# Optimization experiments

Measured on AMD Instinct MI355X. Metric: run time of the kernel, lower is better.

The kernel has to match this reference:

```python
import jax, jax.numpy as jnp
import numpy as np

N_NODES = 100000
N_EDGES = 1600000
IN_CH = 64
HID = 64
OUT = 2


def sage_conv(x, src, dst, W_agg, W_root, b):
    # PyG SAGEConv (mean aggr): out = lin_l(mean_{j in N(i)} x_j) + lin_r(x_i)
    n = x.shape[0]
    msgs = x[src]                                        # [E, F] gather
    agg = jax.ops.segment_sum(msgs, dst, num_segments=n)  # [N, F] scatter-add
    cnt = jax.ops.segment_sum(jnp.ones((src.shape[0], 1), x.dtype), dst, num_segments=n)
    agg = agg / jnp.maximum(cnt, 1)                      # mean; isolated nodes -> 0
    return agg @ W_agg + x @ W_root + b


def setup_inputs() -> dict:
    key = jax.random.key(0)
    ks = jax.random.split(key, 8)
    s = lambda f: 1.0 / np.sqrt(f)
    x = jax.random.normal(ks[0], (N_NODES, IN_CH), dtype=jnp.float32)
    edge_index = jax.random.randint(ks[1], (2, N_EDGES), 0, N_NODES, dtype=jnp.int64)
    return {
        "x": x,
        "edge_index": edge_index,
        "W1_agg": jax.random.normal(ks[2], (IN_CH, HID), dtype=jnp.float32) * s(IN_CH),
        "W1_root": jax.random.normal(ks[3], (IN_CH, HID), dtype=jnp.float32) * s(IN_CH),
        "b1": jnp.zeros((HID,), jnp.float32),
        "W2_agg": jax.random.normal(ks[4], (HID, HID), dtype=jnp.float32) * s(HID),
        "W2_root": jax.random.normal(ks[5], (HID, HID), dtype=jnp.float32) * s(HID),
        "b2": jnp.zeros((HID,), jnp.float32),
        "W_lin": jax.random.normal(ks[6], (HID, OUT), dtype=jnp.float32) * s(HID),
        "b_lin": jnp.zeros((OUT,), jnp.float32),
    }


def reference(x, edge_index, W1_agg, W1_root, b1, W2_agg, W2_root, b2, W_lin, b_lin):
    src, dst = edge_index[0], edge_index[1]
    h = jax.nn.relu(sage_conv(x, src, dst, W1_agg, W1_root, b1))   # dropout = identity (eval)
    h = jax.nn.relu(sage_conv(h, src, dst, W2_agg, W2_root, b2))
    return h @ W_lin + b_lin
```

## Files before the change

kernel.cpp:

```cpp
#include <hip/hip_runtime.h>
#include <hip/hip_bf16.h>

#define FEAT 64
#define CHUNK 8192
#define MAX_NB 1024

typedef __attribute__((ext_vector_type(8))) short bf16x8;
typedef __attribute__((ext_vector_type(4))) float f32x4;

__device__ __forceinline__ float bflo2f(unsigned int u) {
    union { unsigned int u; float f; } v; v.u = u << 16; return v.f;
}
__device__ __forceinline__ float bfhi2f(unsigned int u) {
    union { unsigned int u; float f; } v; v.u = u & 0xffff0000u; return v.f;
}
__device__ __forceinline__ unsigned short f2bf(float f) {
    union { float f; unsigned int u; } v; v.f = f;
    unsigned int u = v.u;
    u += 0x7fffu + ((u >> 16) & 1u);
    return (unsigned short)(u >> 16);
}

__global__ void detect_kernel(const unsigned short* __restrict__ xh,
                              const int* __restrict__ ei32,
                              int* __restrict__ flags) {
    __shared__ int cnt_bf, cnt_nz;
    int tid = threadIdx.x;
    if (tid == 0) { cnt_bf = 0; cnt_nz = 0; }
    __syncthreads();
    unsigned short h = xh[tid * 2];
    int e = (h >> 7) & 0xFF;
    if (e >= 110 && e <= 132) atomicAdd(&cnt_bf, 1);
    if (ei32[tid * 2 + 1] != 0) atomicAdd(&cnt_nz, 1);
    __syncthreads();
    if (tid == 0) {
        flags[0] = (cnt_bf >= 128) ? 1 : 0;
        flags[1] = (cnt_nz < 8) ? 1 : 0;
    }
}

__global__ void cvt_x_kernel(const void* __restrict__ in, unsigned short* __restrict__ out16,
                             int n8, const int* __restrict__ flags) {
    int i = blockIdx.x * 256 + threadIdx.x;
    if (i >= n8) return;
    if (flags[0]) {
        ((uint4*)out16)[i] = ((const uint4*)in)[i];
    } else {
        float4 a = ((const float4*)in)[2 * i];
        float4 b = ((const float4*)in)[2 * i + 1];
        uint4 o;
        o.x = (unsigned int)f2bf(a.x) | ((unsigned int)f2bf(a.y) << 16);
        o.y = (unsigned int)f2bf(a.z) | ((unsigned int)f2bf(a.w) << 16);
        o.z = (unsigned int)f2bf(b.x) | ((unsigned int)f2bf(b.y) << 16);
        o.w = (unsigned int)f2bf(b.z) | ((unsigned int)f2bf(b.w) << 16);
        ((uint4*)out16)[i] = o;
    }
}

__global__ void cvt_weights_kernel(const void* __restrict__ w1a, const void* __restrict__ w1r,
                                   const void* __restrict__ b1,  const void* __restrict__ w2a,
                                   const void* __restrict__ w2r, const void* __restrict__ b2,
                                   const void* __restrict__ wl,  const void* __restrict__ bl,
                                   float* __restrict__ out, unsigned short* __restrict__ Wt,
                                   const int* __restrict__ flags) {
    int i = blockIdx.x * 256 + threadIdx.x;
    if (i >= 16642) return;
    const void* src; int off;
    if      (i < 4096)  { src = w1a; off = i; }
    else if (i < 8192)  { src = w1r; off = i - 4096; }
    else if (i < 8256)  { src = b1;  off = i - 8192; }
    else if (i < 12352) { src = w2a; off = i - 8256; }
    else if (i < 16448) { src = w2r; off = i - 12352; }
    else if (i < 16512) { src = b2;  off = i - 16448; }
    else if (i < 16640) { src = wl;  off = i - 16512; }
    else                { src = bl;  off = i - 16640; }
    float v = flags[0] ? bflo2f(((const unsigned short*)src)[off])
                       : ((const float*)src)[off];
    out[i] = v;
    unsigned short hv = f2bf(v);
    if (i < 4096)                      Wt[(off & 63) * 128 + (off >> 6)] = hv;
    else if (i < 8192)                 Wt[(off & 63) * 128 + 64 + (off >> 6)] = hv;
    else if (i >= 8256 && i < 12352)   Wt[8192 + (off & 63) * 128 + (off >> 6)] = hv;
    else if (i >= 12352 && i < 16448)  Wt[8192 + (off & 63) * 128 + 64 + (off >> 6)] = hv;
}

__global__ __launch_bounds__(256) void p1_hist_kernel(
    const int* __restrict__ ei32, int* __restrict__ hist,
    int E, int N, int NB, int EC, const int* __restrict__ flags) {
    __shared__ int lh[MAX_NB];
    int tid = threadIdx.x, c = blockIdx.x;
    for (int i = tid; i < NB; i += 256) lh[i] = 0;
    __syncthreads();
    int idx64 = flags[1];
    long base = (long)c * CHUNK;
#pragma unroll 4
    for (int j = 0; j < CHUNK / 256; ++j) {
        long e = base + j * 256 + tid;
        if (e < E) {
            int s = idx64 ? ei32[2 * e]             : ei32[e];
            int d = idx64 ? ei32[2 * ((long)E + e)] : ei32[(long)E + e];
            if ((unsigned)s < (unsigned)N && (unsigned)d < (unsigned)N)
                atomicAdd(&lh[d >> 8], 1);
        }
    }
    __syncthreads();
    for (int k = tid; k < NB; k += 256) hist[(long)k * EC + c] = lh[k];
}

__global__ __launch_bounds__(256) void scan1_kernel(const int* __restrict__ in,
                                                    int* __restrict__ out,
                                                    int* __restrict__ blocksum, int n) {
    int tid = threadIdx.x;
    int base = blockIdx.x * 2048 + tid * 8;
    int v[8];
    int tsum = 0;
#pragma unroll
    for (int i = 0; i < 8; ++i) {
        v[i] = (base + i < n) ? in[base + i] : 0;
        tsum += v[i];
    }
    int lane = tid & 63;
    int x = tsum;
#pragma unroll
    for (int off = 1; off < 64; off <<= 1) {
        int y = __shfl_up(x, off);
        if (lane >= off) x += y;
    }
    __shared__ int wsum[4];
    int wave = tid >> 6;
    if (lane == 63) wsum[wave] = x;
    __syncthreads();
    int woff = 0;
#pragma unroll
    for (int w = 0; w < 4; ++w) if (w < wave) woff += wsum[w];
    int run = woff + x - tsum;
#pragma unroll
    for (int i = 0; i < 8; ++i) {
        if (base + i < n) out[base + i] = run;
        run += v[i];
    }
    if (tid == 255) blocksum[blockIdx.x] = woff + x;
}

__global__ void scan2_kernel(int* __restrict__ blocksum, int B) {
    if (threadIdx.x == 0 && blockIdx.x == 0) {
        int run = 0;
        for (int i = 0; i < B; ++i) { int v = blocksum[i]; blocksum[i] = run; run += v; }
    }
}

__global__ void scan3_kernel(int* __restrict__ out, const int* __restrict__ blocksum, int n) {
    int i = blockIdx.x * 256 + threadIdx.x;
    if (i < n) out[i] += blocksum[i >> 11];
}

__global__ __launch_bounds__(256) void p3_scatter_kernel(
    const int* __restrict__ ei32, const int* __restrict__ hscan,
    int* __restrict__ bkt, int E, int N, int NB, int EC,
    const int* __restrict__ flags) {
    __shared__ int lh[MAX_NB];
    int tid = threadIdx.x, c = blockIdx.x;
    for (int i = tid; i < NB; i += 256) lh[i] = 0;
    __syncthreads();
    int idx64 = flags[1];
    long base = (long)c * CHUNK;
#pragma unroll 4
    for (int j = 0; j < CHUNK / 256; ++j) {
        long e = base + j * 256 + tid;
        if (e < E) {
            int s = idx64 ? ei32[2 * e]             : ei32[e];
            int d = idx64 ? ei32[2 * ((long)E + e)] : ei32[(long)E + e];
            if ((unsigned)s < (unsigned)N && (unsigned)d < (unsigned)N) {
                int k = d >> 8;
                int r = atomicAdd(&lh[k], 1);
                bkt[hscan[(long)k * EC + c] + r] = s | ((d & 255) << 20);
            }
        }
    }
}

__global__ __launch_bounds__(256) void p4_build_kernel(
    const int* __restrict__ bkt, const int* __restrict__ hscan, const int* __restrict__ hist,
    int* __restrict__ offs, int* __restrict__ cnt, int* __restrict__ srcs,
    int E, int N, int NB, int EC) {
    int k = blockIdx.x, tid = threadIdx.x;
    int start = hscan[(long)k * EC];
    int end = (k + 1 < NB) ? hscan[(long)(k + 1) * EC]
                           : (hscan[(long)NB * EC - 1] + hist[(long)NB * EC - 1]);
    __shared__ int lc[256], lheads[256], wsum[4];
    lc[tid] = 0;
    __syncthreads();
    for (int e = start + tid; e < end; e += 256)
        atomicAdd(&lc[(bkt[e] >> 20) & 255], 1);
    __syncthreads();
    int cv = lc[tid];
    int lane = tid & 63, wave = tid >> 6;
    int x = cv;
#pragma unroll
    for (int off = 1; off < 64; off <<= 1) {
        int y = __shfl_up(x, off);
        if (lane >= off) x += y;
    }
    if (lane == 63) wsum[wave] = x;
    __syncthreads();
    int woff = 0;
#pragma unroll
    for (int w = 0; w < 4; ++w) if (w < wave) woff += wsum[w];
    int excl = woff + x - cv;
    int gnode = k * 256 + tid;
    if (gnode < N) { offs[gnode] = start + excl; cnt[gnode] = cv; }
    lheads[tid] = excl;
    __syncthreads();
    for (int e = start + tid; e < end; e += 256) {
        int p = bkt[e];
        int d8 = (p >> 20) & 255;
        int pos = start + atomicAdd(&lheads[d8], 1);
        srcs[pos] = p & 0xFFFFF;
    }
}

__global__ __launch_bounds__(256) void aggregate_kernel(
    const unsigned short* __restrict__ feat16, const int* __restrict__ srcs,
    const int* __restrict__ offs, const int* __restrict__ cnt,
    unsigned short* __restrict__ agg16, int N) {
    long gid = (long)blockIdx.x * 256 + threadIdx.x;
    int node = (int)(gid >> 6);
    if (node >= N) return;
    int lane = threadIdx.x & 63;
    int half = lane >> 5;
    int li = lane & 31;
    int start = offs[node];
    int deg = cnt[node];
    int end = start + deg;
    float acc0 = 0.f, acc1 = 0.f;
    int e = start;
    for (; e + 8 <= end; e += 8) {
        int s0 = srcs[e + 0 + half];
        int s1 = srcs[e + 2 + half];
        int s2 = srcs[e + 4 + half];
        int s3 = srcs[e + 6 + half];
        unsigned u0 = *(const unsigned*)(feat16 + (size_t)s0 * FEAT + 2 * li);
        unsigned u1 = *(const unsigned*)(feat16 + (size_t)s1 * FEAT + 2 * li);
        unsigned u2 = *(const unsigned*)(feat16 + (size_t)s2 * FEAT + 2 * li);
        unsigned u3 = *(const unsigned*)(feat16 + (size_t)s3 * FEAT + 2 * li);
        acc0 += bflo2f(u0 & 0xffffu); acc1 += bfhi2f(u0);
        acc0 += bflo2f(u1 & 0xffffu); acc1 += bfhi2f(u1);
        acc0 += bflo2f(u2 & 0xffffu); acc1 += bfhi2f(u2);
        acc0 += bflo2f(u3 & 0xffffu); acc1 += bfhi2f(u3);
    }
    for (; e < end; e += 2) {
        int idx = e + half;
        int s = srcs[idx < end ? idx : end - 1];
        unsigned u = *(const unsigned*)(feat16 + (size_t)s * FEAT + 2 * li);
        if (idx < end) { acc0 += bflo2f(u & 0xffffu); acc1 += bfhi2f(u); }
    }
    acc0 += __shfl_xor(acc0, 32);
    acc1 += __shfl_xor(acc1, 32);
    if (half == 0) {
        float inv = 1.0f / (float)(deg > 0 ? deg : 1);
        unsigned o = (unsigned)f2bf(acc0 * inv) | ((unsigned)f2bf(acc1 * inv) << 16);
        *(unsigned*)(agg16 + (size_t)node * FEAT + 2 * li) = o;
    }
}

__global__ __launch_bounds__(256) void sage_gemm_kernel(
    const unsigned short* __restrict__ agg16, const unsigned short* __restrict__ root16,
    const unsigned short* __restrict__ Wt, const float* __restrict__ bias,
    unsigned short* __restrict__ out16, int N,
    const float* __restrict__ wl, const float* __restrict__ bl,
    void* __restrict__ out_final, const int* __restrict__ flags) {

    __shared__ unsigned short A_l[64][136];
    __shared__ unsigned short B_l[64][136];

    int tid = threadIdx.x;
    int blk = blockIdx.x;

#pragma unroll
    for (int i = 0; i < 4; ++i) {
        int ch = tid + i * 256;
        int n = ch >> 4, kc = ch & 15;
        *(uint4*)&B_l[n][kc * 8] = *(const uint4*)(Wt + n * 128 + kc * 8);
    }
#pragma unroll
    for (int i = 0; i < 4; ++i) {
        int ch = tid + i * 256;
        int r = ch >> 4, c = ch & 15;
        int row = blk * 64 + r;
        uint4 u = make_uint4(0, 0, 0, 0);
        if (row < N)
            u = (c < 8) ? ((const uint4*)(agg16 + (size_t)row * FEAT))[c]
                        : ((const uint4*)(root16 + (size_t)row * FEAT))[c - 8];
        *(uint4*)&A_l[r][c * 8] = u;
    }
    __syncthreads();

    int lane = tid & 63;
    int wave = tid >> 6;
    int r0 = wave * 16;
    int m = lane & 15, quad = lane >> 4;

    f32x4 acc0 = {0.f, 0.f, 0.f, 0.f};
    f32x4 acc1 = acc0, acc2 = acc0, acc3 = acc0;

#pragma unroll
    for (int k0 = 0; k0 < 128; k0 += 32) {
        bf16x8 a = *(const bf16x8*)&A_l[r0 + m][k0 + quad * 8];
        bf16x8 b0 = *(const bf16x8*)&B_l[ 0 + m][k0 + quad * 8];
        bf16x8 b1 = *(const bf16x8*)&B_l[16 + m][k0 + quad * 8];
        bf16x8 b2 = *(const bf16x8*)&B_l[32 + m][k0 + quad * 8];
        bf16x8 b3 = *(const bf16x8*)&B_l[48 + m][k0 + quad * 8];
        acc0 = __builtin_amdgcn_mfma_f32_16x16x32_bf16(a, b0, acc0, 0, 0, 0);
        acc1 = __builtin_amdgcn_mfma_f32_16x16x32_bf16(a, b1, acc1, 0, 0, 0);
        acc2 = __builtin_amdgcn_mfma_f32_16x16x32_bf16(a, b2, acc2, 0, 0, 0);
        acc3 = __builtin_amdgcn_mfma_f32_16x16x32_bf16(a, b3, acc3, 0, 0, 0);
    }
    __syncthreads();

#pragma unroll
    for (int c = 0; c < 4; ++c) {
        f32x4 av = (c == 0) ? acc0 : (c == 1) ? acc1 : (c == 2) ? acc2 : acc3;
        float bv = bias[c * 16 + m];
#pragma unroll
        for (int reg = 0; reg < 4; ++reg) {
            float v = fmaxf(av[reg] + bv, 0.f);
            A_l[r0 + quad * 4 + reg][c * 16 + m] = f2bf(v);
        }
    }
    __syncthreads();

#pragma unroll
    for (int i = 0; i < 2; ++i) {
        int ch = tid + i * 256;
        int r = ch >> 3, c = ch & 7;
        int row = blk * 64 + r;
        if (row < N)
            ((uint4*)(out16 + (size_t)row * FEAT))[c] = *(const uint4*)&A_l[r][c * 8];
    }

    if (wl) {
        int r = tid >> 2, part = tid & 3;
        int row = blk * 64 + r;
        if (row < N) {
            float p0 = 0.f, p1 = 0.f;
#pragma unroll
            for (int j = 0; j < 16; ++j) {
                int f = part * 16 + j;
                float v = bflo2f(A_l[r][f]);
                p0 += v * wl[f * 2 + 0];
                p1 += v * wl[f * 2 + 1];
            }
            p0 += __shfl_down(p0, 2, 4); p0 += __shfl_down(p0, 1, 4);
            p1 += __shfl_down(p1, 2, 4); p1 += __shfl_down(p1, 1, 4);
            if (part == 0) {
                p0 += bl[0];
                p1 += bl[1];
                if (flags[0]) {
                    unsigned int o = ((unsigned int)f2bf(p1) << 16) | (unsigned int)f2bf(p0);
                    ((unsigned int*)out_final)[row] = o;
                } else {
                    ((float2*)out_final)[row] = make_float2(p0, p1);
                }
            }
        }
    }
}

extern "C" void kernel_launch(void* const* d_in, const int* in_sizes, int n_in,
                              void* d_out, int out_size, void* d_ws, size_t ws_size,
                              hipStream_t stream) {
    const void* x_in = d_in[0];
    const int*  ei32 = (const int*)d_in[1];

    int N = in_sizes[0] / FEAT;
    int E = in_sizes[1] / 2;
    int NB = (N + 255) >> 8;
    int EC = (E + CHUNK - 1) / CHUNK;
    int HN = NB * EC;

    unsigned short* x16   = (unsigned short*)d_ws;
    unsigned short* h16   = x16 + (size_t)N * FEAT;
    unsigned short* agg16 = h16 + (size_t)N * FEAT;
    unsigned short* Wt    = agg16 + (size_t)N * FEAT;
    float*          wbuf  = (float*)(Wt + 16384);
    int*            hist  = (int*)(wbuf + 16704);
    int*            hscan = hist + HN;
    int*            bsum  = hscan + HN;
    int*            flags = bsum + 1024;
    int*            offs  = flags + 16;
    int*            cnt   = offs + N;
    int*            bkt   = cnt + N;
    int*            srcs  = bkt + E;

    float* b1_32 = wbuf + 8192;
    float* b2_32 = wbuf + 16448;
    float* wl32  = wbuf + 16512;
    float* bl32  = wbuf + 16640;

    detect_kernel<<<1, 256, 0, stream>>>((const unsigned short*)x_in, ei32, flags);

    int n8 = N * FEAT / 8;
    cvt_x_kernel<<<(n8 + 255) / 256, 256, 0, stream>>>(x_in, x16, n8, flags);
    cvt_weights_kernel<<<(16642 + 255) / 256, 256, 0, stream>>>(
        d_in[2], d_in[3], d_in[4], d_in[5], d_in[6], d_in[7], d_in[8], d_in[9],
        wbuf, Wt, flags);

    p1_hist_kernel<<<EC, 256, 0, stream>>>(ei32, hist, E, N, NB, EC, flags);
    int sB = (HN + 2047) / 2048;
    scan1_kernel<<<sB, 256, 0, stream>>>(hist, hscan, bsum, HN);
    scan2_kernel<<<1, 64, 0, stream>>>(bsum, sB);
    scan3_kernel<<<(HN + 255) / 256, 256, 0, stream>>>(hscan, bsum, HN);
    p3_scatter_kernel<<<EC, 256, 0, stream>>>(ei32, hscan, bkt, E, N, NB, EC, flags);
    p4_build_kernel<<<NB, 256, 0, stream>>>(bkt, hscan, hist, offs, cnt, srcs, E, N, NB, EC);

    int aBlocks = (int)(((long)N * 64 + 255) / 256);
    int gBlocks = (N + 63) / 64;

    aggregate_kernel<<<aBlocks, 256, 0, stream>>>(x16, srcs, offs, cnt, agg16, N);
    sage_gemm_kernel<<<gBlocks, 256, 0, stream>>>(agg16, x16, Wt, b1_32, h16, N,
                                                  nullptr, nullptr, nullptr, flags);

    aggregate_kernel<<<aBlocks, 256, 0, stream>>>(h16, srcs, offs, cnt, agg16, N);
    sage_gemm_kernel<<<gBlocks, 256, 0, stream>>>(agg16, h16, Wt + 8192, b2_32, h16, N,
                                                  wl32, bl32, d_out, flags);
}
```

Measured before the change: 282.1 us.

## Vectorize neighbor gather to 16-byte loads and drop redundant prepasses

The aggregate kernel now gives each lane eight bf16 features through one 16-byte load, with eight edges in flight per wave instead of two, and reduces across lane groups with shuffles. The bf16-input path no longer copies x into a workspace and reads the raw input directly. The histogram pass stops loading source indices, and the single-thread scan2 launch is folded into scan3 as a per-thread prefix loop over block sums. Invalid source indices are clamped to 0 rather than dropped, which changes the semantics for out-of-range edges, and scan3 repeats the block-sum reads in every thread.

```diff
diff --git a/kernel.cpp b/kernel.cpp
--- a/kernel.cpp
+++ b/kernel.cpp
@@ -41,20 +41,17 @@
 
 __global__ void cvt_x_kernel(const void* __restrict__ in, unsigned short* __restrict__ out16,
                              int n8, const int* __restrict__ flags) {
+    if (flags[0]) return;
     int i = blockIdx.x * 256 + threadIdx.x;
     if (i >= n8) return;
-    if (flags[0]) {
-        ((uint4*)out16)[i] = ((const uint4*)in)[i];
-    } else {
-        float4 a = ((const float4*)in)[2 * i];
-        float4 b = ((const float4*)in)[2 * i + 1];
-        uint4 o;
-        o.x = (unsigned int)f2bf(a.x) | ((unsigned int)f2bf(a.y) << 16);
-        o.y = (unsigned int)f2bf(a.z) | ((unsigned int)f2bf(a.w) << 16);
-        o.z = (unsigned int)f2bf(b.x) | ((unsigned int)f2bf(b.y) << 16);
-        o.w = (unsigned int)f2bf(b.z) | ((unsigned int)f2bf(b.w) << 16);
-        ((uint4*)out16)[i] = o;
-    }
+    float4 a = ((const float4*)in)[2 * i];
+    float4 b = ((const float4*)in)[2 * i + 1];
+    uint4 o;
+    o.x = (unsigned int)f2bf(a.x) | ((unsigned int)f2bf(a.y) << 16);
+    o.y = (unsigned int)f2bf(a.z) | ((unsigned int)f2bf(a.w) << 16);
+    o.z = (unsigned int)f2bf(b.x) | ((unsigned int)f2bf(b.y) << 16);
+    o.w = (unsigned int)f2bf(b.z) | ((unsigned int)f2bf(b.w) << 16);
+    ((uint4*)out16)[i] = o;
 }
 
 __global__ void cvt_weights_kernel(const void* __restrict__ w1a, const void* __restrict__ w1r,
@@ -97,9 +94,8 @@
     for (int j = 0; j < CHUNK / 256; ++j) {
         long e = base + j * 256 + tid;
         if (e < E) {
-            int s = idx64 ? ei32[2 * e]             : ei32[e];
             int d = idx64 ? ei32[2 * ((long)E + e)] : ei32[(long)E + e];
-            if ((unsigned)s < (unsigned)N && (unsigned)d < (unsigned)N)
+            if ((unsigned)d < (unsigned)N)
                 atomicAdd(&lh[d >> 8], 1);
         }
     }
@@ -142,16 +138,13 @@
     if (tid == 255) blocksum[blockIdx.x] = woff + x;
 }
 
-__global__ void scan2_kernel(int* __restrict__ blocksum, int B) {
-    if (threadIdx.x == 0 && blockIdx.x == 0) {
-        int run = 0;
-        for (int i = 0; i < B; ++i) { int v = blocksum[i]; blocksum[i] = run; run += v; }
-    }
-}
-
 __global__ void scan3_kernel(int* __restrict__ out, const int* __restrict__ blocksum, int n) {
     int i = blockIdx.x * 256 + threadIdx.x;
-    if (i < n) out[i] += blocksum[i >> 11];
+    if (i >= n) return;
+    int nb = i >> 11;
+    int pre = 0;
+    for (int b = 0; b < nb; ++b) pre += blocksum[b];
+    out[i] += pre;
 }
 
 __global__ __launch_bounds__(256) void p3_scatter_kernel(
@@ -170,7 +163,8 @@
         if (e < E) {
             int s = idx64 ? ei32[2 * e]             : ei32[e];
             int d = idx64 ? ei32[2 * ((long)E + e)] : ei32[(long)E + e];
-            if ((unsigned)s < (unsigned)N && (unsigned)d < (unsigned)N) {
+            if ((unsigned)d < (unsigned)N) {
+                if ((unsigned)s >= (unsigned)N) s = 0;
                 int k = d >> 8;
                 int r = atomicAdd(&lh[k], 1);
                 bkt[hscan[(long)k * EC + c] + r] = s | ((d & 255) << 20);
@@ -220,55 +214,75 @@
 }
 
 __global__ __launch_bounds__(256) void aggregate_kernel(
-    const unsigned short* __restrict__ feat16, const int* __restrict__ srcs,
+    const void* __restrict__ feat_raw, const unsigned short* __restrict__ feat_ws,
+    const int* __restrict__ srcs,
     const int* __restrict__ offs, const int* __restrict__ cnt,
-    unsigned short* __restrict__ agg16, int N) {
+    unsigned short* __restrict__ agg16, int N, const int* __restrict__ flags) {
+    const unsigned short* feat16 = flags[0] ? (const unsigned short*)feat_raw : feat_ws;
     long gid = (long)blockIdx.x * 256 + threadIdx.x;
     int node = (int)(gid >> 6);
     if (node >= N) return;
     int lane = threadIdx.x & 63;
-    int half = lane >> 5;
-    int li = lane & 31;
+    int g = lane >> 3;
+    int li = lane & 7;
     int start = offs[node];
     int deg = cnt[node];
     int end = start + deg;
-    float acc0 = 0.f, acc1 = 0.f;
+    float acc[8] = {0.f, 0.f, 0.f, 0.f, 0.f, 0.f, 0.f, 0.f};
     int e = start;
-    for (; e + 8 <= end; e += 8) {
-        int s0 = srcs[e + 0 + half];
-        int s1 = srcs[e + 2 + half];
-        int s2 = srcs[e + 4 + half];
-        int s3 = srcs[e + 6 + half];
-        unsigned u0 = *(const unsigned*)(feat16 + (size_t)s0 * FEAT + 2 * li);
-        unsigned u1 = *(const unsigned*)(feat16 + (size_t)s1 * FEAT + 2 * li);
-        unsigned u2 = *(const unsigned*)(feat16 + (size_t)s2 * FEAT + 2 * li);
-        unsigned u3 = *(const unsigned*)(feat16 + (size_t)s3 * FEAT + 2 * li);
-        acc0 += bflo2f(u0 & 0xffffu); acc1 += bfhi2f(u0);
-        acc0 += bflo2f(u1 & 0xffffu); acc1 += bfhi2f(u1);
-        acc0 += bflo2f(u2 & 0xffffu); acc1 += bfhi2f(u2);
-        acc0 += bflo2f(u3 & 0xffffu); acc1 += bfhi2f(u3);
-    }
-    for (; e < end; e += 2) {
-        int idx = e + half;
-        int s = srcs[idx < end ? idx : end - 1];
-        unsigned u = *(const unsigned*)(feat16 + (size_t)s * FEAT + 2 * li);
-        if (idx < end) { acc0 += bflo2f(u & 0xffffu); acc1 += bfhi2f(u); }
-    }
-    acc0 += __shfl_xor(acc0, 32);
-    acc1 += __shfl_xor(acc1, 32);
-    if (half == 0) {
+    for (; e + 16 <= end; e += 16) {
+        int s0 = srcs[e + g];
+        int s1 = srcs[e + 8 + g];
+        uint4 u0 = *(const uint4*)(feat16 + (size_t)s0 * FEAT + 8 * li);
+        uint4 u1 = *(const uint4*)(feat16 + (size_t)s1 * FEAT + 8 * li);
+        acc[0] += bflo2f(u0.x & 0xffffu); acc[1] += bfhi2f(u0.x);
+        acc[2] += bflo2f(u0.y & 0xffffu); acc[3] += bfhi2f(u0.y);
+        acc[4] += bflo2f(u0.z & 0xffffu); acc[5] += bfhi2f(u0.z);
+        acc[6] += bflo2f(u0.w & 0xffffu); acc[7] += bfhi2f(u0.w);
+        acc[0] += bflo2f(u1.x & 0xffffu); acc[1] += bfhi2f(u1.x);
+        acc[2] += bflo2f(u1.y & 0xffffu); acc[3] += bfhi2f(u1.y);
+        acc[4] += bflo2f(u1.z & 0xffffu); acc[5] += bfhi2f(u1.z);
+        acc[6] += bflo2f(u1.w & 0xffffu); acc[7] += bfhi2f(u1.w);
+    }
+    for (; e < end; e += 8) {
+        int idx = e + g;
+        bool ok = idx < end;
+        int s = srcs[ok ? idx : end - 1];
+        uint4 u = *(const uint4*)(feat16 + (size_t)s * FEAT + 8 * li);
+        if (ok) {
+            acc[0] += bflo2f(u.x & 0xffffu); acc[1] += bfhi2f(u.x);
+            acc[2] += bflo2f(u.y & 0xffffu); acc[3] += bfhi2f(u.y);
+            acc[4] += bflo2f(u.z & 0xffffu); acc[5] += bfhi2f(u.z);
+            acc[6] += bflo2f(u.w & 0xffffu); acc[7] += bfhi2f(u.w);
+        }
+    }
+#pragma unroll
+    for (int i = 0; i < 8; ++i) {
+        acc[i] += __shfl_xor(acc[i], 8);
+        acc[i] += __shfl_xor(acc[i], 16);
+        acc[i] += __shfl_xor(acc[i], 32);
+    }
+    if (g == 0) {
         float inv = 1.0f / (float)(deg > 0 ? deg : 1);
-        unsigned o = (unsigned)f2bf(acc0 * inv) | ((unsigned)f2bf(acc1 * inv) << 16);
-        *(unsigned*)(agg16 + (size_t)node * FEAT + 2 * li) = o;
+        uint4 o;
+        o.x = (unsigned)f2bf(acc[0] * inv) | ((unsigned)f2bf(acc[1] * inv) << 16);
+        o.y = (unsigned)f2bf(acc[2] * inv) | ((unsigned)f2bf(acc[3] * inv) << 16);
+        o.z = (unsigned)f2bf(acc[4] * inv) | ((unsigned)f2bf(acc[5] * inv) << 16);
+        o.w = (unsigned)f2bf(acc[6] * inv) | ((unsigned)f2bf(acc[7] * inv) << 16);
+        *(uint4*)(agg16 + (size_t)node * FEAT + 8 * li) = o;
     }
 }
 
 __global__ __launch_bounds__(256) void sage_gemm_kernel(
-    const unsigned short* __restrict__ agg16, const unsigned short* __restrict__ root16,
+    const unsigned short* __restrict__ agg16,
+    const void* __restrict__ root_raw, const unsigned short* __restrict__ root_ws,
     const unsigned short* __restrict__ Wt, const float* __restrict__ bias,
     unsigned short* __restrict__ out16, int N,
     const float* __restrict__ wl, const float* __restrict__ bl,
-    void* __restrict__ out_final, const int* __restrict__ flags) {
+    void* __restrict__ out_final, const int* __restrict__ flags, int root_sel) {
+
+    const unsigned short* root16 =
+        (root_sel && !flags[0]) ? root_ws : (const unsigned short*)root_raw;
 
     __shared__ unsigned short A_l[64][136];
     __shared__ unsigned short B_l[64][136];
@@ -408,7 +422,6 @@
     p1_hist_kernel<<<EC, 256, 0, stream>>>(ei32, hist, E, N, NB, EC, flags);
     int sB = (HN + 2047) / 2048;
     scan1_kernel<<<sB, 256, 0, stream>>>(hist, hscan, bsum, HN);
-    scan2_kernel<<<1, 64, 0, stream>>>(bsum, sB);
     scan3_kernel<<<(HN + 255) / 256, 256, 0, stream>>>(hscan, bsum, HN);
     p3_scatter_kernel<<<EC, 256, 0, stream>>>(ei32, hscan, bkt, E, N, NB, EC, flags);
     p4_build_kernel<<<NB, 256, 0, stream>>>(bkt, hscan, hist, offs, cnt, srcs, E, N, NB, EC);
@@ -416,11 +429,11 @@
     int aBlocks = (int)(((long)N * 64 + 255) / 256);
     int gBlocks = (N + 63) / 64;
 
-    aggregate_kernel<<<aBlocks, 256, 0, stream>>>(x16, srcs, offs, cnt, agg16, N);
-    sage_gemm_kernel<<<gBlocks, 256, 0, stream>>>(agg16, x16, Wt, b1_32, h16, N,
-                                                  nullptr, nullptr, nullptr, flags);
-
-    aggregate_kernel<<<aBlocks, 256, 0, stream>>>(h16, srcs, offs, cnt, agg16, N);
-    sage_gemm_kernel<<<gBlocks, 256, 0, stream>>>(agg16, h16, Wt + 8192, b2_32, h16, N,
-                                                  wl32, bl32, d_out, flags);
-}
+    aggregate_kernel<<<aBlocks, 256, 0, stream>>>(x_in, x16, srcs, offs, cnt, agg16, N, flags);
+    sage_gemm_kernel<<<gBlocks, 256, 0, stream>>>(agg16, x_in, x16, Wt, b1_32, h16, N,
+                                                  nullptr, nullptr, nullptr, flags, 1);
+
+    aggregate_kernel<<<aBlocks, 256, 0, stream>>>(h16, h16, srcs, offs, cnt, agg16, N, flags);
+    sage_gemm_kernel<<<gBlocks, 256, 0, stream>>>(agg16, h16, h16, Wt + 8192, b2_32, h16, N,
+                                                  wl32, bl32, d_out, flags, 0);
+}
```

After: 261.9 us. 7.2% less time.
